# Optimization experiments

Measured on AMD Instinct MI355X. Metric: run time of the kernel, lower is better.

Reference implementation:

```python
import jax, jax.numpy as jnp
import numpy as np
import math

DIM = 384
HEADS = 6
HEAD_DIM = DIM // HEADS
MLP_HIDDEN = int(DIM * 2.0)


def layer_norm(x, g, b, eps=1e-5):
    mu = jnp.mean(x, axis=-1, keepdims=True)
    var = jnp.mean((x - mu) ** 2, axis=-1, keepdims=True)
    return (x - mu) * jax.lax.rsqrt(var + eps) * g + b


def setup_inputs() -> dict:
    key = jax.random.key(0)
    ks = jax.random.split(key, 12)
    B, N = 4, 2048
    s = 0.02
    return {
        "x": jax.random.normal(ks[0], (B, N, DIM), dtype=jnp.float32),
        "pos": jax.random.normal(ks[1], (B, N, 3), dtype=jnp.float32),
        "qkv_w": jax.random.normal(ks[2], (DIM, 3 * DIM), dtype=jnp.float32) * s,
        "qkv_b": jnp.zeros((3 * DIM,), jnp.float32),
        "proj_w": jax.random.normal(ks[3], (DIM, DIM), dtype=jnp.float32) * s,
        "proj_b": jnp.zeros((DIM,), jnp.float32),
        "mlp_w1": jax.random.normal(ks[4], (DIM, MLP_HIDDEN), dtype=jnp.float32) * s,
        "mlp_b1": jnp.zeros((MLP_HIDDEN,), jnp.float32),
        "mlp_w2": jax.random.normal(ks[5], (MLP_HIDDEN, DIM), dtype=jnp.float32) * s,
        "mlp_b2": jnp.zeros((DIM,), jnp.float32),
        "ln1_g": jnp.ones((DIM,), jnp.float32),
        "ln1_b": jnp.zeros((DIM,), jnp.float32),
        "ln2_g": jnp.ones((DIM,), jnp.float32),
        "ln2_b": jnp.zeros((DIM,), jnp.float32),
    }


def reference(x, pos, qkv_w, qkv_b, proj_w, proj_b, mlp_w1, mlp_b1,
              mlp_w2, mlp_b2, ln1_g, ln1_b, ln2_g, ln2_b):
    B, N, D = x.shape
    H, Hd = HEADS, HEAD_DIM
    # qkv projection
    qkv = layer_norm(x, ln1_g, ln1_b) @ qkv_w + qkv_b          # [B,N,3D]
    qkv = qkv.reshape(B, N, 3, H, Hd)
    q = jnp.transpose(qkv[:, :, 0], (0, 2, 1, 3))               # [B,H,N,Hd]
    k = jnp.transpose(qkv[:, :, 1], (0, 2, 1, 3))
    v = jnp.transpose(qkv[:, :, 2], (0, 2, 1, 3))
    # pairwise squared-distance bias: exp(-||p_i - p_j||^2)
    rel = pos[:, :, None, :] - pos[:, None, :, :]               # [B,N,N,3]
    dist = jnp.exp(-jnp.sum(rel ** 2, axis=-1))                 # [B,N,N]
    scale = 1.0 / math.sqrt(Hd)
    attn = jnp.einsum('bhqd,bhkd->bhqk', q, k) * scale + dist[:, None, :, :]
    attn = jax.nn.softmax(attn, axis=-1)
    out = jnp.einsum('bhqk,bhkd->bhqd', attn, v)                # [B,H,N,Hd]
    out = jnp.transpose(out, (0, 2, 1, 3)).reshape(B, N, D)
    out = out @ proj_w + proj_b
    x = x + out
    h = layer_norm(x, ln2_g, ln2_b)
    h = jax.nn.gelu(h @ mlp_w1 + mlp_b1, approximate=False) @ mlp_w2 + mlp_b2
    return x + h
```

## Files before the change

kernel.cpp:

```cpp
#include <hip/hip_runtime.h>
#include <hip/hip_bf16.h>
#include <math.h>

#define DIMD 384
#define NHEADS 6
#define HD 64
#define MLPH 768
#define SEQ 2048
#define NBATCH 4
#define NTOK (NBATCH*SEQ)

typedef __hip_bfloat16 bf16;

typedef __attribute__((ext_vector_type(8))) short bf16x8;
typedef __attribute__((ext_vector_type(4))) float f32x4;

#define LOG2E 1.44269504088896340736f

static __device__ inline float fexp2(float x) { return __builtin_amdgcn_exp2f(x); }

static __device__ inline f32x4 mfma16(bf16x8 a, bf16x8 b, f32x4 c) {
    return __builtin_amdgcn_mfma_f32_16x16x32_bf16(a, b, c, 0, 0, 0);
}

static __device__ inline unsigned int cvtpk(float lo, float hi) {
    unsigned int r;
    asm("v_cvt_pk_bf16_f32 %0, %1, %2" : "=v"(r) : "v"(lo), "v"(hi));
    return r;
}
static __device__ inline float bflo(unsigned int u) { return __builtin_bit_cast(float, u << 16); }
static __device__ inline float bfhi(unsigned int u) { return __builtin_bit_cast(float, u & 0xffff0000u); }

static __device__ inline void gld16(const void* g, void* l) {
    __builtin_amdgcn_global_load_lds(
        (const __attribute__((address_space(1))) unsigned int*)g,
        (__attribute__((address_space(3))) unsigned int*)l, 16, 0, 0);
}

__global__ __launch_bounds__(256) void ln_k(const float* __restrict__ x,
                                            const float* __restrict__ gm,
                                            const float* __restrict__ bt,
                                            bf16* __restrict__ out) {
    int row = blockIdx.x * 4 + (threadIdx.x >> 6);
    int l = threadIdx.x & 63;
    const float* xr = x + (size_t)row * DIMD;
    float v[6];
#pragma unroll
    for (int j = 0; j < 6; ++j) v[j] = xr[l + 64 * j];
    float s = 0.f, s2 = 0.f;
#pragma unroll
    for (int j = 0; j < 6; ++j) { s += v[j]; s2 += v[j] * v[j]; }
#pragma unroll
    for (int m = 1; m < 64; m <<= 1) { s += __shfl_xor(s, m); s2 += __shfl_xor(s2, m); }
    float mu = s * (1.f / DIMD);
    float var = s2 * (1.f / DIMD) - mu * mu;
    float rs = rsqrtf(var + 1e-5f);
    bf16* orow = out + (size_t)row * DIMD;
#pragma unroll
    for (int j = 0; j < 6; ++j) {
        int i = l + 64 * j;
        orow[i] = __float2bfloat16((v[j] - mu) * rs * gm[i] + bt[i]);
    }
}

__global__ __launch_bounds__(256) void wtrans_k(const float* __restrict__ W,
                                                bf16* __restrict__ WT,
                                                int K, int N) {
    __shared__ float t[32][33];
    int tx = threadIdx.x & 31, ty = threadIdx.x >> 5;
    int nb = blockIdx.x * 32, kb = blockIdx.y * 32;
#pragma unroll
    for (int i = 0; i < 4; ++i)
        t[ty + 8 * i][tx] = W[(size_t)(kb + ty + 8 * i) * N + nb + tx];
    __syncthreads();
#pragma unroll
    for (int i = 0; i < 4; ++i)
        WT[(size_t)(nb + ty + 8 * i) * K + kb + tx] = __float2bfloat16(t[tx][ty + 8 * i]);
}

__global__ __launch_bounds__(256) void vtrans_k(const bf16* __restrict__ v_,
                                                bf16* __restrict__ vT_) {
    const unsigned short* v = (const unsigned short*)v_;
    unsigned short* vT = (unsigned short*)vT_;
    __shared__ unsigned short t[32][33];
    int tx = threadIdx.x & 31, ty = threadIdx.x >> 5;
    int nb = blockIdx.x * 32, db = blockIdx.y * 32;
    int bh = blockIdx.z;
    const unsigned short* src = v + (size_t)bh * SEQ * HD;
#pragma unroll
    for (int i = 0; i < 4; ++i)
        t[ty + 8 * i][tx] = src[(size_t)(nb + ty + 8 * i) * HD + db + tx];
    __syncthreads();
    unsigned short* dst = vT + (size_t)bh * HD * SEQ;
#pragma unroll
    for (int i = 0; i < 4; ++i)
        dst[(size_t)(db + ty + 8 * i) * SEQ + nb + tx] = t[tx][ty + 8 * i];
}

__global__ __launch_bounds__(256) void dist_k(const float* __restrict__ pos,
                                              bf16* __restrict__ DP) {
    int blk = blockIdx.x;
    int w = blk & 3, qt = (blk >> 2) & 31, b = blk >> 7;
    int l = threadIdx.x & 63, tt = threadIdx.x >> 6;
    int lq = l & 15, g = l >> 4;
    int q = qt * 64 + w * 16 + lq;
    const float* pq = pos + ((size_t)b * SEQ + q) * 3;
    float px = pq[0], py = pq[1], pz = pq[2];
    const float* posb = pos + (size_t)b * SEQ * 3;
    char* base = (char*)DP + (size_t)blk * 65536;
    for (int j = 0; j < 8; ++j) {
        int t = tt * 8 + j;
#pragma unroll
        for (int m = 0; m < 2; ++m) {
            int k0 = t * 64 + 32 * m + 4 * g;
            float a[24];
            const float* pk = posb + 3 * k0;
            *(f32x4*)&a[0]  = *(const f32x4*)pk;
            *(f32x4*)&a[4]  = *(const f32x4*)(pk + 4);
            *(f32x4*)&a[8]  = *(const f32x4*)(pk + 8);
            const float* pk2 = posb + 3 * (k0 + 16);
            *(f32x4*)&a[12] = *(const f32x4*)pk2;
            *(f32x4*)&a[16] = *(const f32x4*)(pk2 + 4);
            *(f32x4*)&a[20] = *(const f32x4*)(pk2 + 8);
            float o8[8];
#pragma unroll
            for (int r = 0; r < 8; ++r) {
                float dx = px - a[3 * r], dy = py - a[3 * r + 1], dz = pz - a[3 * r + 2];
                o8[r] = fexp2(-LOG2E * (dx * dx + dy * dy + dz * dz)) * LOG2E;
            }
            uint4 o;
            o.x = cvtpk(o8[0], o8[1]); o.y = cvtpk(o8[2], o8[3]);
            o.z = cvtpk(o8[4], o8[5]); o.w = cvtpk(o8[6], o8[7]);
            *(uint4*)(base + ((size_t)t * 2 + m) * 1024 + l * 16) = o;
        }
    }
}

template <int EPI>
__global__ __launch_bounds__(256) void gemm128_k(const bf16* __restrict__ A,
                                                 const bf16* __restrict__ WT,
                                                 const float* __restrict__ bias,
                                                 bf16* __restrict__ ob0,
                                                 bf16* __restrict__ ob1,
                                                 bf16* __restrict__ ob2,
                                                 int K, int Nw) {
    __shared__ __align__(16) char Als[2][8192];
    __shared__ __align__(16) char Bls[2][8192];
    int tid = threadIdx.x;
    int w = tid >> 6, l = tid & 63;
    int c = l & 15, g = l >> 4;
    int wr = w >> 1, wc = w & 1;
    int m0 = blockIdx.y * 128, n0 = blockIdx.x * 128;
    const char* Ag = (const char*)A + (size_t)m0 * K * 2;
    const char* Bg = (const char*)WT + (size_t)n0 * K * 2;
    int K2 = K * 2;

    f32x4 acc[4][4];
#pragma unroll
    for (int mi = 0; mi < 4; ++mi)
#pragma unroll
        for (int ni = 0; ni < 4; ++ni) acc[mi][ni] = (f32x4){0.f, 0.f, 0.f, 0.f};

    auto stage = [&](int t, int bi) {
#pragma unroll
        for (int p = 0; p < 2; ++p) {
            int chunk = p * 256 + tid;
            int r = chunk >> 2;
            int cc = ((chunk & 3) ^ (r & 3)) << 4;
            gld16(Ag + (size_t)r * K2 + t * 64 + cc, &Als[bi][chunk * 16]);
            gld16(Bg + (size_t)r * K2 + t * 64 + cc, &Bls[bi][chunk * 16]);
        }
    };

    stage(0, 0);
    int kcn = K >> 5;
    for (int t = 0; t < kcn; ++t) {
        int bi = t & 1;
        __syncthreads();
        if (t + 1 < kcn) stage(t + 1, bi ^ 1);
        bf16x8 af[4], bfr[4];
#pragma unroll
        for (int mi = 0; mi < 4; ++mi) {
            int row = wr * 64 + mi * 16 + c;
            __builtin_memcpy(&af[mi], &Als[bi][row * 64 + ((g ^ (row & 3)) << 4)], 16);
        }
#pragma unroll
        for (int ni = 0; ni < 4; ++ni) {
            int row = wc * 64 + ni * 16 + c;
            __builtin_memcpy(&bfr[ni], &Bls[bi][row * 64 + ((g ^ (row & 3)) << 4)], 16);
        }
#pragma unroll
        for (int mi = 0; mi < 4; ++mi)
#pragma unroll
            for (int ni = 0; ni < 4; ++ni)
                acc[mi][ni] = mfma16(af[mi], bfr[ni], acc[mi][ni]);
    }

#pragma unroll
    for (int mi = 0; mi < 4; ++mi) {
#pragma unroll
        for (int ni = 0; ni < 4; ++ni) {
            int ntb = n0 + wc * 64 + ni * 16;
#pragma unroll
            for (int r = 0; r < 4; ++r) {
                int m = m0 + wr * 64 + mi * 16 + 4 * g + r;
                int n = ntb + c;
                float val = acc[mi][ni][r] + bias[n];
                if (EPI == 0) {
                    int which = ntb / DIMD;
                    int rem = ntb - which * DIMD;
                    int h = rem >> 6;
                    int d = (rem & 63) + c;
                    int b = m >> 11, s = m & (SEQ - 1);
                    bf16* dp = which == 0 ? ob0 : (which == 1 ? ob1 : ob2);
                    dp[(((size_t)b * NHEADS + h) * SEQ + s) * HD + d] = __float2bfloat16(val);
                } else {
                    float ge = 0.5f * val * (1.0f + erff(val * 0.70710678118654752f));
                    ob0[(size_t)m * Nw + n] = __float2bfloat16(ge);
                }
            }
        }
    }
}

template <int EPI>
__global__ __launch_bounds__(256) void gemm_k(const bf16* __restrict__ A,
                                              const bf16* __restrict__ WT,
                                              const float* __restrict__ bias,
                                              const float* __restrict__ resid,
                                              float* __restrict__ outf,
                                              int K, int Nw) {
    __shared__ __align__(16) char Als[2][8192];
    __shared__ __align__(16) char Bls[2][8192];
    int tid = threadIdx.x;
    int w = tid >> 6, l = tid & 63;
    int c = l & 15, g = l >> 4;
    int m0 = blockIdx.y * 64, n0 = blockIdx.x * 64;
    const char* Ag = (const char*)A + (size_t)m0 * K * 2;
    const char* Bg = (const char*)WT + (size_t)n0 * K * 2;
    int K2 = K * 2;

    f32x4 acc[4];
#pragma unroll
    for (int nt = 0; nt < 4; ++nt) acc[nt] = (f32x4){0.f, 0.f, 0.f, 0.f};

    auto stage = [&](int t, int bi) {
#pragma unroll
        for (int p = 0; p < 2; ++p) {
            int chunk = p * 256 + tid;
            int r = chunk >> 3;
            int cc = ((chunk & 7) ^ (r & 7)) << 4;
            gld16(Ag + (size_t)r * K2 + t * 128 + cc, &Als[bi][chunk * 16]);
            gld16(Bg + (size_t)r * K2 + t * 128 + cc, &Bls[bi][chunk * 16]);
        }
    };

    stage(0, 0);
    int kcn = K >> 6;
    int arow = (16 * w + c) * 128;
    int sw = c & 7;
    for (int t = 0; t < kcn; ++t) {
        int bi = t & 1;
        __syncthreads();
        if (t + 1 < kcn) stage(t + 1, bi ^ 1);
#pragma unroll
        for (int kk = 0; kk < 2; ++kk) {
            int ch = ((kk * 4 + g) ^ sw) << 4;
            bf16x8 af;
            __builtin_memcpy(&af, &Als[bi][arow + ch], 16);
#pragma unroll
            for (int nt = 0; nt < 4; ++nt) {
                bf16x8 bfr;
                __builtin_memcpy(&bfr, &Bls[bi][(nt * 16 + c) * 128 + ch], 16);
                acc[nt] = mfma16(af, bfr, acc[nt]);
            }
        }
    }

#pragma unroll
    for (int nt = 0; nt < 4; ++nt) {
        int ntb = n0 + nt * 16;
#pragma unroll
        for (int r = 0; r < 4; ++r) {
            int m = m0 + 16 * w + 4 * g + r;
            int n = ntb + c;
            float val = acc[nt][r] + bias[n];
            val += resid[(size_t)m * Nw + n];
            outf[(size_t)m * Nw + n] = val;
        }
    }
}

__global__ __launch_bounds__(256) void attn_k(const bf16* __restrict__ q,
                                              const bf16* __restrict__ k,
                                              const bf16* __restrict__ vT,
                                              const bf16* __restrict__ DP,
                                              bf16* __restrict__ out) {
    __shared__ __align__(16) char Kls[2][8192];
    __shared__ __align__(16) char Vls[2][8192];
    __shared__ __align__(16) unsigned int P_lds[4][16][20];

    int tid = threadIdx.x;
    int w = tid >> 6, l = tid & 63;
    int lq = l & 15, g = l >> 4;
    int qt = blockIdx.x & 31;
    int bh = blockIdx.x >> 5;
    int b = bh / NHEADS, h = bh % NHEADS;
    int qrow = qt * 64 + w * 16 + lq;

    const bf16* qp = q + ((size_t)bh * SEQ + qrow) * HD + 8 * g;
    bf16x8 qf0 = *(const bf16x8*)qp;
    bf16x8 qf1 = *(const bf16x8*)(qp + 32);

    const char* kgb = (const char*)(k + (size_t)bh * SEQ * HD);
    const char* vgb = (const char*)(vT + (size_t)bh * HD * SEQ);
    const char* dpb = (const char*)DP + ((size_t)((b * 32 + qt) * 4 + w)) * 65536 + l * 16;

    const float SC2 = 0.125f * LOG2E;
    float lloc = 0.f;
    f32x4 oacc[4];
#pragma unroll
    for (int dt = 0; dt < 4; ++dt) oacc[dt] = (f32x4){0.f, 0.f, 0.f, 0.f};

    auto stage = [&](int t, int bi) {
#pragma unroll
        for (int p = 0; p < 2; ++p) {
            int chunk = p * 256 + tid;
            int r = chunk >> 3, c = chunk & 7;
            int cc = (c ^ (r & 7)) << 4;
            gld16(kgb + (size_t)t * 8192 + r * 128 + cc, &Kls[bi][chunk * 16]);
            gld16(vgb + (size_t)r * 4096 + t * 128 + cc, &Vls[bi][chunk * 16]);
        }
    };

    stage(0, 0);
    uint4 cdp0 = *(const uint4*)(dpb);
    uint4 cdp1 = *(const uint4*)(dpb + 1024);

    int swq = lq & 7;
    for (int t = 0; t < 32; ++t) {
        int bi = t & 1;
        __syncthreads();
        uint4 ndp0 = {0, 0, 0, 0}, ndp1 = {0, 0, 0, 0};
        if (t + 1 < 32) {
            stage(t + 1, bi ^ 1);
            const char* dpn = dpb + (size_t)(t + 1) * 2048;
            ndp0 = *(const uint4*)(dpn);
            ndp1 = *(const uint4*)(dpn + 1024);
        }

        f32x4 st[4];
#pragma unroll
        for (int s = 0; s < 4; ++s) {
            int ro = (16 * s + lq) * 128;
            bf16x8 klo, khi;
            __builtin_memcpy(&klo, &Kls[bi][ro + ((g ^ swq) << 4)], 16);
            __builtin_memcpy(&khi, &Kls[bi][ro + (((4 + g) ^ swq) << 4)], 16);
            f32x4 z = (f32x4){0.f, 0.f, 0.f, 0.f};
            st[s] = mfma16(klo, qf0, z);
            st[s] = mfma16(khi, qf1, st[s]);
        }

#pragma unroll
        for (int m = 0; m < 2; ++m) {
            uint4 cd = m == 0 ? cdp0 : cdp1;
            f32x4 s0v = st[2 * m], s1v = st[2 * m + 1];
            float p[8];
            p[0] = fexp2(s0v[0] * SC2 + bflo(cd.x));
            p[1] = fexp2(s0v[1] * SC2 + bfhi(cd.x));
            p[2] = fexp2(s0v[2] * SC2 + bflo(cd.y));
            p[3] = fexp2(s0v[3] * SC2 + bfhi(cd.y));
            p[4] = fexp2(s1v[0] * SC2 + bflo(cd.z));
            p[5] = fexp2(s1v[1] * SC2 + bfhi(cd.z));
            p[6] = fexp2(s1v[2] * SC2 + bflo(cd.w));
            p[7] = fexp2(s1v[3] * SC2 + bfhi(cd.w));
#pragma unroll
            for (int i = 0; i < 8; ++i) lloc += p[i];

            P_lds[w][lq][2 * g] = cvtpk(p[0], p[1]);
            P_lds[w][lq][2 * g + 1] = cvtpk(p[2], p[3]);
            P_lds[w][lq][8 + 2 * g] = cvtpk(p[4], p[5]);
            P_lds[w][lq][8 + 2 * g + 1] = cvtpk(p[6], p[7]);
            bf16x8 pf;
            __builtin_memcpy(&pf, &P_lds[w][lq][4 * g], 16);

#pragma unroll
            for (int dt = 0; dt < 4; ++dt) {
                int rv = (16 * dt + lq) * 128;
                bf16x8 vf;
                __builtin_memcpy(&vf, &Vls[bi][rv + (((4 * m + g) ^ swq) << 4)], 16);
                oacc[dt] = mfma16(vf, pf, oacc[dt]);
            }
        }
        cdp0 = ndp0; cdp1 = ndp1;
    }

    float lrun = lloc;
    lrun += __shfl_xor(lrun, 16);
    lrun += __shfl_xor(lrun, 32);
    float inv = 1.f / lrun;
    bf16* op = out + ((size_t)b * SEQ + qrow) * DIMD + h * HD + 4 * g;
#pragma unroll
    for (int dt = 0; dt < 4; ++dt) {
        unsigned int t2[2];
        t2[0] = cvtpk(oacc[dt][0] * inv, oacc[dt][1] * inv);
        t2[1] = cvtpk(oacc[dt][2] * inv, oacc[dt][3] * inv);
        __builtin_memcpy(op + dt * 16, t2, 8);
    }
}

extern "C" void kernel_launch(void* const* d_in, const int* in_sizes, int n_in,
                              void* d_out, int out_size, void* d_ws, size_t ws_size,
                              hipStream_t stream) {
    const float* x      = (const float*)d_in[0];
    const float* pos    = (const float*)d_in[1];
    const float* qkv_w  = (const float*)d_in[2];
    const float* qkv_b  = (const float*)d_in[3];
    const float* proj_w = (const float*)d_in[4];
    const float* proj_b = (const float*)d_in[5];
    const float* mlp_w1 = (const float*)d_in[6];
    const float* mlp_b1 = (const float*)d_in[7];
    const float* mlp_w2 = (const float*)d_in[8];
    const float* mlp_b2 = (const float*)d_in[9];
    const float* ln1_g  = (const float*)d_in[10];
    const float* ln1_b  = (const float*)d_in[11];
    const float* ln2_g  = (const float*)d_in[12];
    const float* ln2_b  = (const float*)d_in[13];

    char* p = (char*)d_ws;
    size_t off = 0;
    auto alloc = [&](size_t bytes) {
        char* r = p + off;
        off = (off + bytes + 255) & ~(size_t)255;
        return r;
    };
    bf16* WT1 = (bf16*)alloc((size_t)1152 * 384 * 2);
    bf16* WT2 = (bf16*)alloc((size_t)384 * 384 * 2);
    bf16* WT3 = (bf16*)alloc((size_t)384 * 768 * 2);
    bf16* WT4 = (bf16*)alloc((size_t)768 * 384 * 2);
    bf16* xn  = (bf16*)alloc((size_t)NTOK * DIMD * 2);
    bf16* xn2 = (bf16*)alloc((size_t)NTOK * DIMD * 2);
    bf16* qb  = (bf16*)alloc((size_t)NTOK * DIMD * 2);
    bf16* kb  = (bf16*)alloc((size_t)NTOK * DIMD * 2);
    bf16* vb  = (bf16*)alloc((size_t)NTOK * DIMD * 2);
    bf16* vTb = (bf16*)alloc((size_t)NTOK * DIMD * 2);
    bf16* ao  = (bf16*)alloc((size_t)NTOK * DIMD * 2);
    float* x1 = (float*)alloc((size_t)NTOK * DIMD * 4);
    bf16* hh  = (bf16*)alloc((size_t)NTOK * MLPH * 2);
    bf16* dtab = (bf16*)alloc((size_t)NBATCH * SEQ * SEQ * 2);
    if (off > ws_size) return;

    wtrans_k<<<dim3(36, 12), 256, 0, stream>>>(qkv_w, WT1, 384, 1152);
    wtrans_k<<<dim3(12, 12), 256, 0, stream>>>(proj_w, WT2, 384, 384);
    wtrans_k<<<dim3(24, 12), 256, 0, stream>>>(mlp_w1, WT3, 384, 768);
    wtrans_k<<<dim3(12, 24), 256, 0, stream>>>(mlp_w2, WT4, 768, 384);

    dist_k<<<NBATCH * 32 * 4, 256, 0, stream>>>(pos, dtab);

    ln_k<<<NTOK / 4, 256, 0, stream>>>(x, ln1_g, ln1_b, xn);
    gemm128_k<0><<<dim3(1152 / 128, NTOK / 128), 256, 0, stream>>>(
        xn, WT1, qkv_b, qb, kb, vb, 384, 1152);
    vtrans_k<<<dim3(SEQ / 32, HD / 32, NBATCH * NHEADS), 256, 0, stream>>>(vb, vTb);
    attn_k<<<NBATCH * NHEADS * (SEQ / 64), 256, 0, stream>>>(qb, kb, vTb, dtab, ao);
    gemm_k<1><<<dim3(384 / 64, NTOK / 64), 256, 0, stream>>>(
        ao, WT2, proj_b, x, x1, 384, 384);
    ln_k<<<NTOK / 4, 256, 0, stream>>>(x1, ln2_g, ln2_b, xn2);
    gemm128_k<2><<<dim3(768 / 128, NTOK / 128), 256, 0, stream>>>(
        xn2, WT3, mlp_b1, hh, nullptr, nullptr, 384, 768);
    gemm_k<3><<<dim3(384 / 64, NTOK / 64), 256, 0, stream>>>(
        hh, WT4, mlp_b2, x1, (float*)d_out, 768, 384);
}
```

Measured before the change: 152.9 us.

## Permute V transpose layout to keep P in registers; merge weight transposes

The V transpose kernel now writes key columns in a permuted order that matches the register layout of the exponentiated scores. The attention kernel can then feed P straight from registers into the MFMA, with no round trip through LDS. This removes LDS writes and reads in the inner loop. Separately, the four weight-transpose launches are merged into one kernel that picks its matrix by block index, cutting launch overhead.

```diff
diff --git a/kernel.cpp b/kernel.cpp
--- a/kernel.cpp
+++ b/kernel.cpp
@@ -63,19 +63,31 @@
     }
 }
 
-__global__ __launch_bounds__(256) void wtrans_k(const float* __restrict__ W,
-                                                bf16* __restrict__ WT,
-                                                int K, int N) {
+__global__ __launch_bounds__(256) void wtransall_k(const float* __restrict__ w1,
+                                                   const float* __restrict__ w2,
+                                                   const float* __restrict__ w3,
+                                                   const float* __restrict__ w4,
+                                                   bf16* __restrict__ o1,
+                                                   bf16* __restrict__ o2,
+                                                   bf16* __restrict__ o3,
+                                                   bf16* __restrict__ o4) {
     __shared__ float t[32][33];
+    int id = blockIdx.x;
+    const float* W; bf16* O; int K, N;
+    if (id < 432)      { W = w1; O = o1; K = 384; N = 1152; }
+    else if (id < 576) { W = w2; O = o2; K = 384; N = 384;  id -= 432; }
+    else if (id < 864) { W = w3; O = o3; K = 384; N = 768;  id -= 576; }
+    else               { W = w4; O = o4; K = 768; N = 384;  id -= 864; }
+    int nbx = N >> 5;
+    int nb = (id % nbx) * 32, kb = (id / nbx) * 32;
     int tx = threadIdx.x & 31, ty = threadIdx.x >> 5;
-    int nb = blockIdx.x * 32, kb = blockIdx.y * 32;
 #pragma unroll
     for (int i = 0; i < 4; ++i)
         t[ty + 8 * i][tx] = W[(size_t)(kb + ty + 8 * i) * N + nb + tx];
     __syncthreads();
 #pragma unroll
     for (int i = 0; i < 4; ++i)
-        WT[(size_t)(nb + ty + 8 * i) * K + kb + tx] = __float2bfloat16(t[tx][ty + 8 * i]);
+        O[(size_t)(nb + ty + 8 * i) * K + kb + tx] = __float2bfloat16(t[tx][ty + 8 * i]);
 }
 
 __global__ __launch_bounds__(256) void vtrans_k(const bf16* __restrict__ v_,
@@ -92,9 +104,10 @@
         t[ty + 8 * i][tx] = src[(size_t)(nb + ty + 8 * i) * HD + db + tx];
     __syncthreads();
     unsigned short* dst = vT + (size_t)bh * HD * SEQ;
+    int pc = 8 * ((tx & 15) >> 2) + 4 * (tx >> 4) + (tx & 3);
 #pragma unroll
     for (int i = 0; i < 4; ++i)
-        dst[(size_t)(db + ty + 8 * i) * SEQ + nb + tx] = t[tx][ty + 8 * i];
+        dst[(size_t)(db + ty + 8 * i) * SEQ + nb + pc] = t[tx][ty + 8 * i];
 }
 
 __global__ __launch_bounds__(256) void dist_k(const float* __restrict__ pos,
@@ -298,7 +311,6 @@
                                               bf16* __restrict__ out) {
     __shared__ __align__(16) char Kls[2][8192];
     __shared__ __align__(16) char Vls[2][8192];
-    __shared__ __align__(16) unsigned int P_lds[4][16][20];
 
     int tid = threadIdx.x;
     int w = tid >> 6, l = tid & 63;
@@ -377,12 +389,13 @@
 #pragma unroll
             for (int i = 0; i < 8; ++i) lloc += p[i];
 
-            P_lds[w][lq][2 * g] = cvtpk(p[0], p[1]);
-            P_lds[w][lq][2 * g + 1] = cvtpk(p[2], p[3]);
-            P_lds[w][lq][8 + 2 * g] = cvtpk(p[4], p[5]);
-            P_lds[w][lq][8 + 2 * g + 1] = cvtpk(p[6], p[7]);
+            unsigned int pw[4];
+            pw[0] = cvtpk(p[0], p[1]);
+            pw[1] = cvtpk(p[2], p[3]);
+            pw[2] = cvtpk(p[4], p[5]);
+            pw[3] = cvtpk(p[6], p[7]);
             bf16x8 pf;
-            __builtin_memcpy(&pf, &P_lds[w][lq][4 * g], 16);
+            __builtin_memcpy(&pf, pw, 16);
 
 #pragma unroll
             for (int dt = 0; dt < 4; ++dt) {
@@ -450,10 +463,8 @@
     bf16* dtab = (bf16*)alloc((size_t)NBATCH * SEQ * SEQ * 2);
     if (off > ws_size) return;
 
-    wtrans_k<<<dim3(36, 12), 256, 0, stream>>>(qkv_w, WT1, 384, 1152);
-    wtrans_k<<<dim3(12, 12), 256, 0, stream>>>(proj_w, WT2, 384, 384);
-    wtrans_k<<<dim3(24, 12), 256, 0, stream>>>(mlp_w1, WT3, 384, 768);
-    wtrans_k<<<dim3(12, 24), 256, 0, stream>>>(mlp_w2, WT4, 768, 384);
+    wtransall_k<<<1152, 256, 0, stream>>>(qkv_w, proj_w, mlp_w1, mlp_w2,
+                                          WT1, WT2, WT3, WT4);
 
     dist_k<<<NBATCH * 32 * 4, 256, 0, stream>>>(pos, dtab);
 
```

Result: faster. 144.3 us (-5.7%).
